# Performance work log

Hardware: AMD Instinct MI355X
Metric: run time of the kernel (lower is better)

Reference implementation:

```python
import jax, jax.numpy as jnp
import numpy as np

FULL_SCALE = 256
THRESH = 15.0  # full_scale > 128 -> distance_threshold = 15


def bilinear_sample(img, x, y):
    # img: [C,Hi,Wi]; x,y: [...] in [-1,1]; align_corners=False, zero padding
    C, Hi, Wi = img.shape
    xg = ((x + 1.0) * Wi - 1.0) / 2.0
    yg = ((y + 1.0) * Hi - 1.0) / 2.0
    x0 = jnp.floor(xg).astype(jnp.int32); x1 = x0 + 1
    y0 = jnp.floor(yg).astype(jnp.int32); y1 = y0 + 1
    wx = xg - x0.astype(img.dtype); wy = yg - y0.astype(img.dtype)

    def gather(yi, xi):
        valid = (yi >= 0) & (yi < Hi) & (xi >= 0) & (xi < Wi)
        yc = jnp.clip(yi, 0, Hi - 1); xc = jnp.clip(xi, 0, Wi - 1)
        return img[:, yc, xc] * valid[None].astype(img.dtype)

    return (gather(y0, x0) * ((1 - wy) * (1 - wx))[None]
            + gather(y0, x1) * ((1 - wy) * wx)[None]
            + gather(y1, x0) * (wy * (1 - wx))[None]
            + gather(y1, x1) * (wy * wx)[None])  # [C, ...]


def setup_inputs() -> dict:
    key = jax.random.key(0)
    k1, k2 = jax.random.split(key)
    image_x = jax.random.normal(k1, (1, 64, 256, 256), dtype=jnp.float32)
    all_edges = jax.random.uniform(k2, (8, 32, 4), dtype=jnp.float32)
    return {"image_x": image_x, "all_edges": all_edges}


def reference(image_x, all_edges):
    H = W = FULL_SCALE
    rows = jnp.arange(H, dtype=image_x.dtype)
    cols = jnp.arange(W, dtype=image_x.dtype)
    Vs, Us = jnp.meshgrid(rows, cols, indexing='ij')
    UV = jnp.stack([Vs, Us], axis=-1)  # [H,W,2] as (row, col), matches torch UVs

    def per_group(edges):
        e = edges * FULL_SCALE
        e0, e1 = e[:, :2], e[:, 2:4]
        d = e1 - e0                                    # [E,2]
        L = jnp.sqrt((d * d).sum(-1))                  # [E]
        dn = d / jnp.maximum(L, 1e-4)[:, None]
        nrm = jnp.stack([dn[:, 1], -dn[:, 0]], -1)     # normals
        diff = UV[:, :, None, :] - e0                  # [H,W,E,2]
        nd = jnp.abs((diff * nrm).sum(-1))             # normal distances [H,W,E]
        dd = (diff * dn).sum(-1) / jnp.maximum(L, 1e-4)  # direction distances
        near0 = jnp.sqrt((diff * diff).sum(-1)) <= THRESH
        near1 = jnp.sqrt(((UV[:, :, None, :] - e1) ** 2).sum(-1)) <= THRESH
        m = ((nd <= THRESH) & (dd <= 1) & (dd >= 0)) | near0 | near1  # all_edge_mask
        edge_mask = m.any(-1)                          # [H,W]
        off = jnp.minimum(dd, 1.0 - dd)                # point offsets
        mf = m.astype(image_x.dtype)
        pinfo = (off * mf).sum(-1) / jnp.maximum(mf.sum(-1), 1e-4)  # [H,W]
        return edge_mask, pinfo

    edge_mask, pinfo = jax.vmap(per_group)(all_edges)  # [G,H,W], [G,H,W]

    # grid_sample at every grid point (dense/masked equivalent of nonzero+gather);
    # torch swaps (v,u)->(u,v) so x = col, y = row, normalized p/size*2-1
    gx = (Us / FULL_SCALE) * 2.0 - 1.0
    gy = (Vs / FULL_SCALE) * 2.0 - 1.0
    sampled = bilinear_sample(image_x[0], gx, gy)      # [C,H,W]
    sampled = jnp.moveaxis(sampled, 0, -1)             # [H,W,C]

    G = all_edges.shape[0]
    feats = jnp.concatenate(
        [jnp.broadcast_to(sampled, (G,) + sampled.shape), pinfo[..., None]], axis=-1)
    feats = feats * edge_mask[..., None].astype(feats.dtype)  # zero non-edge pixels
    return feats, edge_mask
```

## Files before the change

### kernel.cpp

```cpp
#include <hip/hip_runtime.h>

#define HH 256
#define WW 256
#define CC 64
#define NG 8
#define NE 32
#define PX 32
#define THRESH 15.0f

#define FEATS_ELEMS ((size_t)NG * HH * WW * 65)

#define IMG_ELEMS (CC * 2 * 33)

__global__ __launch_bounds__(256, 5) void fused_sparse_encoder(
    const float* __restrict__ img,
    const float* __restrict__ edges,
    float* __restrict__ out)
{
#pragma clang fp contract(off)
    __shared__ float s_buf[66 * 65];
    __shared__ float s_e0v[NG * NE], s_e0u[NG * NE];
    __shared__ float s_e1v[NG * NE], s_e1u[NG * NE];
    __shared__ float s_dn0[NG * NE], s_dn1[NG * NE], s_Lm[NG * NE];
    __shared__ float s_mask[NG * PX];
    __shared__ float s_pinfo[NG * PX];

    const int tid = threadIdx.x;
    const int u0  = blockIdx.x * PX;
    const int v   = blockIdx.y;

    {
        const float4 e4 = reinterpret_cast<const float4*>(edges)[tid];
        float e0v = e4.x * 256.0f;
        float e0u = e4.y * 256.0f;
        float e1v = e4.z * 256.0f;
        float e1u = e4.w * 256.0f;
        float d0 = e1v - e0v;
        float d1 = e1u - e0u;
        float L  = __fsqrt_rn(d0 * d0 + d1 * d1);
        float Lm = fmaxf(L, 1e-4f);
        s_e0v[tid] = e0v; s_e0u[tid] = e0u;
        s_e1v[tid] = e1v; s_e1u[tid] = e1u;
        s_dn0[tid] = __fdiv_rn(d0, Lm);
        s_dn1[tid] = __fdiv_rn(d1, Lm);
        s_Lm[tid]  = Lm;
    }
    __syncthreads();

    float cbuf[17];
    #pragma unroll
    for (int t = 0; t < 17; ++t) {
        const int i = tid + t * 256;
        float val = 0.0f;
        if (i < IMG_ELEMS) {
            const int c  = i / 66;
            const int r  = i - c * 66;
            const int yy = r / 33;
            const int x  = r - yy * 33;
            const int gy = v - 1 + yy;
            const int gx = u0 - 1 + x;
            if (gy >= 0 && gx >= 0) {
                val = img[((size_t)c * HH + gy) * WW + gx];
            }
        }
        cbuf[t] = val;
    }

    {
        const int px = tid & (PX - 1);
        const int g  = tid >> 5;
        const float U = (float)(u0 + px);
        const float V = (float)v;
        float sm = 0.0f, cnt = 0.0f;
        bool any = false;
        for (int e = 0; e < NE; ++e) {
            const int idx = g * NE + e;
            const float diff0 = V - s_e0v[idx];
            const float diff1 = U - s_e0u[idx];
            const float dn0 = s_dn0[idx];
            const float dn1 = s_dn1[idx];
            const float nd = fabsf(diff0 * dn1 + diff1 * (-dn0));
            const float dd = __fdiv_rn(diff0 * dn0 + diff1 * dn1, s_Lm[idx]);
            const float r0 = __fsqrt_rn(diff0 * diff0 + diff1 * diff1);
            const float f0 = V - s_e1v[idx];
            const float f1 = U - s_e1u[idx];
            const float r1 = __fsqrt_rn(f0 * f0 + f1 * f1);
            const bool m = ((nd <= THRESH) && (dd <= 1.0f) && (dd >= 0.0f))
                           || (r0 <= THRESH) || (r1 <= THRESH);
            if (m) {
                any = true;
                sm += fminf(dd, 1.0f - dd);
                cnt += 1.0f;
            }
        }
        const float pf = __fdiv_rn(sm, fmaxf(cnt, 1e-4f));
        const float mv = any ? 1.0f : 0.0f;
        s_mask[g * PX + px]  = mv;
        s_pinfo[g * PX + px] = pf;
        out[FEATS_ELEMS + ((size_t)g * HH + v) * WW + (u0 + px)] = mv;
    }

    #pragma unroll
    for (int t = 0; t < 17; ++t) {
        const int i = tid + t * 256;
        if (i < IMG_ELEMS) {
            const int c  = i / 66;
            const int r  = i - c * 66;
            const int yy = r / 33;
            const int x  = r - yy * 33;
            s_buf[(yy * 33 + x) * 65 + c] = cbuf[t];
        }
    }
    __syncthreads();

    const int wv   = tid >> 6;
    const int lane = tid & 63;
    float sreg[8];
    #pragma unroll
    for (int i = 0; i < 8; ++i) {
        const int p = wv * 8 + i;
        sreg[i] = s_buf[(p) * 65 + lane] * 0.25f
                + s_buf[(p + 1) * 65 + lane] * 0.25f
                + s_buf[(33 + p) * 65 + lane] * 0.25f
                + s_buf[(34 + p) * 65 + lane] * 0.25f;
    }
    __syncthreads();

    #pragma unroll
    for (int i = 0; i < 8; ++i) {
        const int p = wv * 8 + i;
        s_buf[p * 65 + lane] = sreg[i];
    }
    __syncthreads();

    for (int g = 0; g < NG; ++g) {
        const float* msk = &s_mask[g * PX];
        const float* pin = &s_pinfo[g * PX];
        float* gout = out + (((size_t)g * HH + v) * WW + u0) * 65;
        #pragma unroll
        for (int k = 0; k < 3; ++k) {
            const int q = tid + k * 256;
            if (q < 520) {
                const int f  = q * 4;
                const int p0 = (int)((unsigned)f / 65u);
                const int b  = (p0 + 1) * 65 - f;
                const float4 tv = *reinterpret_cast<const float4*>(&s_buf[f]);
                const float m0  = msk[p0];
                const float m1  = msk[(b < 4) ? (p0 + 1) : p0];
                const float pi0 = pin[p0];
                float r0 = ((b == 1) ? pi0 : tv.x) * ((0 < b) ? m0 : m1);
                float r1 = ((b == 2) ? pi0 : tv.y) * ((1 < b) ? m0 : m1);
                float r2 = ((b == 3) ? pi0 : tv.z) * ((2 < b) ? m0 : m1);
                float r3 = ((b == 4) ? pi0 : tv.w) * ((3 < b) ? m0 : m1);
                *reinterpret_cast<float4*>(&gout[f]) = make_float4(r0, r1, r2, r3);
            }
        }
    }
}

extern "C" void kernel_launch(void* const* d_in, const int* in_sizes, int n_in,
                              void* d_out, int out_size, void* d_ws, size_t ws_size,
                              hipStream_t stream) {
    const float* img   = (const float*)d_in[0];
    const float* edges = (const float*)d_in[1];
    float* out = (float*)d_out;
    dim3 grid(WW / PX, HH);
    fused_sparse_encoder<<<grid, 256, 0, stream>>>(img, edges, out);
}
```

Baseline: 40.84 us.

## Pack edge constants, drop sqrt in distance tests, use nontemporal stores

Packs the per-edge constants into float4/float2/float shared arrays so the inner loop issues fewer LDS loads. The endpoint-distance tests now compare squared distances against 225 instead of taking square roots. The large feature output is written with nontemporal stores to reduce cache pollution, and launch bounds raise the target occupancy from 5 to 6 blocks per SM. Comparing squared distances can flip borderline cases relative to sqrt-then-compare, and the higher occupancy target may constrain registers.

```diff
diff --git a/kernel.cpp b/kernel.cpp
--- a/kernel.cpp
+++ b/kernel.cpp
@@ -8,22 +8,24 @@
 #define PX 32
 #define THRESH 15.0f
 
+typedef float f32x4 __attribute__((ext_vector_type(4)));
+
 #define FEATS_ELEMS ((size_t)NG * HH * WW * 65)
 
 #define IMG_ELEMS (CC * 2 * 33)
 
-__global__ __launch_bounds__(256, 5) void fused_sparse_encoder(
+__global__ __launch_bounds__(256, 6) void fused_sparse_encoder(
     const float* __restrict__ img,
     const float* __restrict__ edges,
     float* __restrict__ out)
 {
 #pragma clang fp contract(off)
-    __shared__ float s_buf[66 * 65];
-    __shared__ float s_e0v[NG * NE], s_e0u[NG * NE];
-    __shared__ float s_e1v[NG * NE], s_e1u[NG * NE];
-    __shared__ float s_dn0[NG * NE], s_dn1[NG * NE], s_Lm[NG * NE];
-    __shared__ float s_mask[NG * PX];
-    __shared__ float s_pinfo[NG * PX];
+    __shared__ float  s_buf[66 * 65];
+    __shared__ float4 s_k1[NG * NE];
+    __shared__ float2 s_k2[NG * NE];
+    __shared__ float  s_k3[NG * NE];
+    __shared__ float  s_mask[NG * PX];
+    __shared__ float  s_pinfo[NG * PX];
 
     const int tid = threadIdx.x;
     const int u0  = blockIdx.x * PX;
@@ -31,19 +33,17 @@
 
     {
         const float4 e4 = reinterpret_cast<const float4*>(edges)[tid];
-        float e0v = e4.x * 256.0f;
-        float e0u = e4.y * 256.0f;
-        float e1v = e4.z * 256.0f;
-        float e1u = e4.w * 256.0f;
-        float d0 = e1v - e0v;
-        float d1 = e1u - e0u;
-        float L  = __fsqrt_rn(d0 * d0 + d1 * d1);
-        float Lm = fmaxf(L, 1e-4f);
-        s_e0v[tid] = e0v; s_e0u[tid] = e0u;
-        s_e1v[tid] = e1v; s_e1u[tid] = e1u;
-        s_dn0[tid] = __fdiv_rn(d0, Lm);
-        s_dn1[tid] = __fdiv_rn(d1, Lm);
-        s_Lm[tid]  = Lm;
+        const float e0v = e4.x * 256.0f;
+        const float e0u = e4.y * 256.0f;
+        const float e1v = e4.z * 256.0f;
+        const float e1u = e4.w * 256.0f;
+        const float d0 = e1v - e0v;
+        const float d1 = e1u - e0u;
+        const float L  = __fsqrt_rn(d0 * d0 + d1 * d1);
+        const float Lm = fmaxf(L, 1e-4f);
+        s_k1[tid] = make_float4(e0v, e0u, __fdiv_rn(d0, Lm), __fdiv_rn(d1, Lm));
+        s_k2[tid] = make_float2(e1v, e1u);
+        s_k3[tid] = Lm;
     }
     __syncthreads();
 
@@ -75,18 +75,20 @@
         bool any = false;
         for (int e = 0; e < NE; ++e) {
             const int idx = g * NE + e;
-            const float diff0 = V - s_e0v[idx];
-            const float diff1 = U - s_e0u[idx];
-            const float dn0 = s_dn0[idx];
-            const float dn1 = s_dn1[idx];
-            const float nd = fabsf(diff0 * dn1 + diff1 * (-dn0));
-            const float dd = __fdiv_rn(diff0 * dn0 + diff1 * dn1, s_Lm[idx]);
-            const float r0 = __fsqrt_rn(diff0 * diff0 + diff1 * diff1);
-            const float f0 = V - s_e1v[idx];
-            const float f1 = U - s_e1u[idx];
-            const float r1 = __fsqrt_rn(f0 * f0 + f1 * f1);
-            const bool m = ((nd <= THRESH) && (dd <= 1.0f) && (dd >= 0.0f))
-                           || (r0 <= THRESH) || (r1 <= THRESH);
+            const float4 k1 = s_k1[idx];
+            const float2 k2 = s_k2[idx];
+            const float  Lm = s_k3[idx];
+            const float diff0 = V - k1.x;
+            const float diff1 = U - k1.y;
+            const float ndv = diff0 * k1.w - diff1 * k1.z;
+            const float ddn = diff0 * k1.z + diff1 * k1.w;
+            const float dd  = __fdiv_rn(ddn, Lm);
+            const float r0sq = diff0 * diff0 + diff1 * diff1;
+            const float f0 = V - k2.x;
+            const float f1 = U - k2.y;
+            const float r1sq = f0 * f0 + f1 * f1;
+            const bool m = ((fabsf(ndv) <= THRESH) && (dd <= 1.0f) && (dd >= 0.0f))
+                           || (r0sq <= 225.0f) || (r1sq <= 225.0f);
             if (m) {
                 any = true;
                 sm += fminf(dd, 1.0f - dd);
@@ -148,11 +150,12 @@
                 const float m0  = msk[p0];
                 const float m1  = msk[(b < 4) ? (p0 + 1) : p0];
                 const float pi0 = pin[p0];
-                float r0 = ((b == 1) ? pi0 : tv.x) * ((0 < b) ? m0 : m1);
-                float r1 = ((b == 2) ? pi0 : tv.y) * ((1 < b) ? m0 : m1);
-                float r2 = ((b == 3) ? pi0 : tv.z) * ((2 < b) ? m0 : m1);
-                float r3 = ((b == 4) ? pi0 : tv.w) * ((3 < b) ? m0 : m1);
-                *reinterpret_cast<float4*>(&gout[f]) = make_float4(r0, r1, r2, r3);
+                f32x4 r;
+                r.x = ((b == 1) ? pi0 : tv.x) * ((0 < b) ? m0 : m1);
+                r.y = ((b == 2) ? pi0 : tv.y) * ((1 < b) ? m0 : m1);
+                r.z = ((b == 3) ? pi0 : tv.z) * ((2 < b) ? m0 : m1);
+                r.w = ((b == 4) ? pi0 : tv.w) * ((3 < b) ? m0 : m1);
+                __builtin_nontemporal_store(r, reinterpret_cast<f32x4*>(&gout[f]));
             }
         }
     }
```

After: 40.39 us. Within noise of the previous version (-1.1%).
